# Kernel optimization log

Hardware: AMD Instinct MI355X
Metric: run time of the kernel (lower is better)

The kernel has to match this reference:

```python
import jax, jax.numpy as jnp
import numpy as np

N = 50000      # nodes
E = 800000     # edges (before self-loops)
F_IN = 64      # num_features
HID = 32       # hidden_channels
HEADS = 4
CLS = 3
NEG_SLOPE = 0.2  # PyG GATConv default


def setup_inputs() -> dict:
    key = jax.random.key(0)
    ks = jax.random.split(key, 12)
    s = 0.1
    return {
        "x": jax.random.normal(ks[0], (N, F_IN), jnp.float32),
        "W1": jax.random.normal(ks[1], (F_IN, HEADS * HID), jnp.float32) * s,
        "att_src1": jax.random.normal(ks[2], (HEADS, HID), jnp.float32) * s,
        "att_dst1": jax.random.normal(ks[3], (HEADS, HID), jnp.float32) * s,
        "b1": jnp.zeros((HEADS * HID,), jnp.float32),
        "W2": jax.random.normal(ks[4], (HEADS * HID, HID), jnp.float32) * s,
        "att_src2": jax.random.normal(ks[5], (1, HID), jnp.float32) * s,
        "att_dst2": jax.random.normal(ks[6], (1, HID), jnp.float32) * s,
        "b2": jnp.zeros((HID,), jnp.float32),
        "linW": jax.random.normal(ks[7], (HID, CLS), jnp.float32) * s,
        "linb": jnp.zeros((CLS,), jnp.float32),
        "edge_index": jax.random.randint(ks[8], (2, E), 0, N, dtype=jnp.int64),
    }


def _gat_conv(x, W, att_src, att_dst, bias, src, dst, heads):
    """PyG GATConv (eval mode, self-loops pre-added in src/dst)."""
    n = x.shape[0]
    h = (x @ W).reshape(n, heads, -1)                      # [N,H,C]
    a_src = jnp.sum(h * att_src, axis=-1)                  # [N,H]
    a_dst = jnp.sum(h * att_dst, axis=-1)                  # [N,H]
    e = jax.nn.leaky_relu(a_src[src] + a_dst[dst], NEG_SLOPE)  # [E,H]
    # segment softmax over destination node
    m = jax.ops.segment_max(e, dst, num_segments=n)
    p = jnp.exp(e - m[dst])
    denom = jax.ops.segment_sum(p, dst, num_segments=n)
    alpha = p / denom[dst]                                 # [E,H]
    msg = h[src] * alpha[:, :, None]                       # [E,H,C]
    out = jax.ops.segment_sum(msg, dst, num_segments=n)    # [N,H,C]
    return out.reshape(n, -1) + bias                       # concat heads


def reference(x, W1, att_src1, att_dst1, b1, W2, att_src2, att_dst2, b2, linW, linb, edge_index):
    n = x.shape[0]
    loop = jnp.arange(n, dtype=edge_index.dtype)
    src = jnp.concatenate([edge_index[0], loop])  # add self-loops (PyG default)
    dst = jnp.concatenate([edge_index[1], loop])
    h = _gat_conv(x, W1, att_src1, att_dst1, b1, src, dst, HEADS)
    h = jax.nn.elu(h)
    h = _gat_conv(h, W2, att_src2, att_dst2, b2, src, dst, 1)
    g = jnp.mean(h, axis=0, keepdims=True)        # batch is None path
    logits = g @ linW + linb                      # [1, CLS]
    return jax.nn.softmax(logits, axis=1)
```

## Files before the change

### kernel.cpp

```cpp
#include <hip/hip_runtime.h>
#include <hip/hip_fp16.h>
#include <math.h>

#define NEG_SLOPE 0.2f
#define CAP 64
#define SCB 2048

static __device__ __forceinline__ void atomAdd(float* a, float v) {
    unsafeAtomicAdd(a, v);
}

static __device__ __forceinline__ bool edges_are_i64(const int* __restrict__ ei) {
    return (ei[1] | ei[3] | ei[5] | ei[7]) == 0;
}
static __device__ __forceinline__ int ldsrc(const int* __restrict__ ei, int e, int E, bool i64) {
    return i64 ? ei[2 * e] : ei[e];
}
static __device__ __forceinline__ int lddst(const int* __restrict__ ei, int e, int E, bool i64) {
    return i64 ? ei[2 * (E + e)] : ei[E + e];
}

__global__ __launch_bounds__(256) void scatter_k(const int* __restrict__ ei,
                                                 int* __restrict__ deg,
                                                 int* __restrict__ col, int E, int N) {
    const int tid = threadIdx.x;
    const int grp = blockIdx.x & 3;
    const int bin = blockIdx.x >> 2;
    const int nb  = gridDim.x >> 2;
    const bool i64 = edges_are_i64(ei);
    const int ET = E + N;
    const int d0 = (int)((long long)grp * N / 4);
    const int d1 = (int)((long long)(grp + 1) * N / 4);
    for (int e = bin * 256 + tid; e < ET; e += nb * 256) {
        int s, d;
        if (e < E) { s = ldsrc(ei, e, E, i64); d = lddst(ei, e, E, i64); }
        else       { s = d = e - E; }
        if (d >= d0 && d < d1) {
            int pos = atomicAdd(&deg[d], 1);
            if (pos < CAP) col[d * CAP + pos] = s;
        }
    }
}

__global__ __launch_bounds__(256, 4) void gemm1_k(const float* __restrict__ x,
                                                  const float* __restrict__ W,
                                                  const float* __restrict__ aws,
                                                  const float* __restrict__ awd,
                                                  __half* __restrict__ h,
                                                  float* __restrict__ as_,
                                                  float* __restrict__ ad_, int N) {
    __shared__ float Ws[64 * 128];
    __shared__ float xs[32 * 64];
    const int tid = threadIdx.x;
    const int cg = tid & 31, rg = tid >> 5;
    const int r0 = blockIdx.x * 32;
#pragma unroll 1
    for (int i = tid; i < 8192; i += 256) Ws[i] = W[i];
    {
        const float* src = x + (size_t)r0 * 64;
        const int limit = (N - r0) * 64;
#pragma unroll 1
        for (int i = tid * 4; i < 2048; i += 1024) {
            float4 v = (i < limit) ? *(const float4*)(src + i) : make_float4(0, 0, 0, 0);
            *(float4*)(xs + i) = v;
        }
    }
    __syncthreads();

    float acc[4][4] = {};
#pragma unroll 2
    for (int k = 0; k < 64; k += 4) {
        float4 w0 = *(const float4*)(Ws + (k + 0) * 128 + cg * 4);
        float4 w1 = *(const float4*)(Ws + (k + 1) * 128 + cg * 4);
        float4 w2 = *(const float4*)(Ws + (k + 2) * 128 + cg * 4);
        float4 w3 = *(const float4*)(Ws + (k + 3) * 128 + cg * 4);
        float4 xv[4];
#pragma unroll
        for (int q = 0; q < 4; ++q) xv[q] = *(const float4*)(xs + (rg * 4 + q) * 64 + k);
#pragma unroll
        for (int q = 0; q < 4; ++q) {
            float4 xq = xv[q];
            acc[q][0] += xq.x * w0.x + xq.y * w1.x + xq.z * w2.x + xq.w * w3.x;
            acc[q][1] += xq.x * w0.y + xq.y * w1.y + xq.z * w2.y + xq.w * w3.y;
            acc[q][2] += xq.x * w0.z + xq.y * w1.z + xq.z * w2.z + xq.w * w3.z;
            acc[q][3] += xq.x * w0.w + xq.y * w1.w + xq.z * w2.w + xq.w * w3.w;
        }
    }

    const int jbase = cg * 4;
    const int head = cg >> 3;
    const float a0 = aws[jbase], a1 = aws[jbase + 1], a2 = aws[jbase + 2], a3 = aws[jbase + 3];
    const float d0 = awd[jbase], d1 = awd[jbase + 1], d2 = awd[jbase + 2], d3 = awd[jbase + 3];
    float ps[4], pd[4];
#pragma unroll
    for (int q = 0; q < 4; ++q) {
        ps[q] = acc[q][0] * a0 + acc[q][1] * a1 + acc[q][2] * a2 + acc[q][3] * a3;
        pd[q] = acc[q][0] * d0 + acc[q][1] * d1 + acc[q][2] * d2 + acc[q][3] * d3;
        int row = r0 + rg * 4 + q;
        if (row < N) {
            __half hv[4];
            hv[0] = __float2half(acc[q][0]); hv[1] = __float2half(acc[q][1]);
            hv[2] = __float2half(acc[q][2]); hv[3] = __float2half(acc[q][3]);
            *(uint2*)(h + (size_t)row * 128 + jbase) = *(uint2*)hv;
        }
    }
#pragma unroll
    for (int off = 4; off; off >>= 1) {
#pragma unroll
        for (int q = 0; q < 4; ++q) {
            ps[q] += __shfl_down(ps[q], off, 8);
            pd[q] += __shfl_down(pd[q], off, 8);
        }
    }
    if ((cg & 7) == 0) {
#pragma unroll
        for (int q = 0; q < 4; ++q) {
            int row = r0 + rg * 4 + q;
            if (row < N) { as_[row * 4 + head] = ps[q]; ad_[row * 4 + head] = pd[q]; }
        }
    }
}

__global__ __launch_bounds__(256, 4) void gemm2_k(const float* __restrict__ hact,
                                                  const float* __restrict__ W,
                                                  const float* __restrict__ aws,
                                                  const float* __restrict__ awd,
                                                  __half* __restrict__ h2,
                                                  float* __restrict__ as_,
                                                  float* __restrict__ ad_, int N) {
    __shared__ float Ws[128 * 32];
    __shared__ float xs[128 * 68];
    const int tid = threadIdx.x;
    const int cg = tid & 7, rg = tid >> 3;
    const int r0 = blockIdx.x * 128;
    for (int i = tid; i < 4096; i += 256) Ws[i] = W[i];

    float acc[4][4] = {};
#pragma unroll 1
    for (int p = 0; p < 2; ++p) {
        __syncthreads();
#pragma unroll 2
        for (int i = tid * 4; i < 8192; i += 1024) {
            int row = i >> 6, kk = i & 63;
            float4 v = (r0 + row < N)
                ? *(const float4*)(hact + (size_t)(r0 + row) * 128 + p * 64 + kk)
                : make_float4(0, 0, 0, 0);
            *(float4*)(xs + row * 68 + kk) = v;
        }
        __syncthreads();
#pragma unroll 2
        for (int k = 0; k < 64; k += 4) {
            float4 w0 = *(const float4*)(Ws + (p * 64 + k + 0) * 32 + cg * 4);
            float4 w1 = *(const float4*)(Ws + (p * 64 + k + 1) * 32 + cg * 4);
            float4 w2 = *(const float4*)(Ws + (p * 64 + k + 2) * 32 + cg * 4);
            float4 w3 = *(const float4*)(Ws + (p * 64 + k + 3) * 32 + cg * 4);
            float4 xv[4];
#pragma unroll
            for (int q = 0; q < 4; ++q) xv[q] = *(const float4*)(xs + (rg * 4 + q) * 68 + k);
#pragma unroll
            for (int q = 0; q < 4; ++q) {
                float4 xq = xv[q];
                acc[q][0] += xq.x * w0.x + xq.y * w1.x + xq.z * w2.x + xq.w * w3.x;
                acc[q][1] += xq.x * w0.y + xq.y * w1.y + xq.z * w2.y + xq.w * w3.y;
                acc[q][2] += xq.x * w0.z + xq.y * w1.z + xq.z * w2.z + xq.w * w3.z;
                acc[q][3] += xq.x * w0.w + xq.y * w1.w + xq.z * w2.w + xq.w * w3.w;
            }
        }
    }

    const int jbase = cg * 4;
    const float a0 = aws[jbase], a1 = aws[jbase + 1], a2 = aws[jbase + 2], a3 = aws[jbase + 3];
    const float d0 = awd[jbase], d1 = awd[jbase + 1], d2 = awd[jbase + 2], d3 = awd[jbase + 3];
    float ps[4], pd[4];
#pragma unroll
    for (int q = 0; q < 4; ++q) {
        ps[q] = acc[q][0] * a0 + acc[q][1] * a1 + acc[q][2] * a2 + acc[q][3] * a3;
        pd[q] = acc[q][0] * d0 + acc[q][1] * d1 + acc[q][2] * d2 + acc[q][3] * d3;
        int row = r0 + rg * 4 + q;
        if (row < N) {
            __half hv[4];
            hv[0] = __float2half(acc[q][0]); hv[1] = __float2half(acc[q][1]);
            hv[2] = __float2half(acc[q][2]); hv[3] = __float2half(acc[q][3]);
            *(uint2*)(h2 + (size_t)row * 32 + jbase) = *(uint2*)hv;
        }
    }
#pragma unroll
    for (int off = 4; off; off >>= 1) {
#pragma unroll
        for (int q = 0; q < 4; ++q) {
            ps[q] += __shfl_down(ps[q], off, 8);
            pd[q] += __shfl_down(pd[q], off, 8);
        }
    }
    if (cg == 0) {
#pragma unroll
        for (int q = 0; q < 4; ++q) {
            int row = r0 + rg * 4 + q;
            if (row < N) { as_[row] = ps[q]; ad_[row] = pd[q]; }
        }
    }
}

__global__ __launch_bounds__(256) void pull_agg1_k(const int* __restrict__ deg,
                                                   const int* __restrict__ col,
                                                   const float* __restrict__ asrc,
                                                   const float* __restrict__ adst,
                                                   const __half* __restrict__ h,
                                                   const float* __restrict__ b1,
                                                   float* __restrict__ hact, int N) {
    int wave = (blockIdx.x * 256 + threadIdx.x) >> 6;
    int lane = threadIdx.x & 63;
    if (wave >= N) return;
    const int d = wave;
    const int hd = lane >> 4;
    const int el = lane & 15;
    const float ad = adst[d * 4 + hd];
    const int* cl = col + d * CAP;
    int cnt = deg[d]; if (cnt > CAP) cnt = CAP;
    float acc0 = 0.0f, acc1 = 0.0f, den = 0.0f;

    for (int i = 0; i < cnt; i += 16) {
        const int r = cnt - i;
        int s = 0; float p = 0.0f;
        if (el < r) {
            s = cl[i + el];
            float v = asrc[s * 4 + hd] + ad;
            v = v > 0.0f ? v : NEG_SLOPE * v;
            p = __expf(v);
        }
        den += p;
        int su[16];
#pragma unroll
        for (int u = 0; u < 16; ++u) su[u] = __shfl(s, u, 16);
        __half2 g[16];
#pragma unroll
        for (int u = 0; u < 16; ++u) g[u] = *(const __half2*)(h + (size_t)su[u] * 128 + lane * 2);
        float pu[16];
#pragma unroll
        for (int u = 0; u < 16; ++u) pu[u] = __shfl(p, u, 16);
#pragma unroll
        for (int u = 0; u < 16; ++u) {
            float2 gf = __half22float2(g[u]);
            acc0 += pu[u] * gf.x; acc1 += pu[u] * gf.y;
        }
    }
    den += __shfl_xor(den, 1, 16);
    den += __shfl_xor(den, 2, 16);
    den += __shfl_xor(den, 4, 16);
    den += __shfl_xor(den, 8, 16);

    float inv = 1.0f / den;
    float o0 = acc0 * inv + b1[lane * 2];
    float o1 = acc1 * inv + b1[lane * 2 + 1];
    o0 = o0 > 0.0f ? o0 : expm1f(o0);
    o1 = o1 > 0.0f ? o1 : expm1f(o1);
    *(float2*)(hact + (size_t)d * 128 + lane * 2) = make_float2(o0, o1);
}

__global__ __launch_bounds__(256) void pull_agg2_k(const int* __restrict__ deg,
                                                   const int* __restrict__ col,
                                                   const float* __restrict__ asrc,
                                                   const float* __restrict__ adst,
                                                   const __half* __restrict__ h,
                                                   float* __restrict__ gsum, int N) {
    const int lane = threadIdx.x & 31;
    const int el = lane & 15;
    const int gloc = threadIdx.x >> 5;
    float csum = 0.0f;
    for (int d = blockIdx.x * 8 + gloc; d < N; d += gridDim.x * 8) {
        const float ad = adst[d];
        const int* cl = col + d * CAP;
        int cnt = deg[d]; if (cnt > CAP) cnt = CAP;
        float acc = 0.0f, den = 0.0f;
        for (int i = 0; i < cnt; i += 16) {
            const int r = cnt - i;
            int s = 0; float p = 0.0f;
            if (el < r) {
                s = cl[i + el];
                float v = asrc[s] + ad;
                v = v > 0.0f ? v : NEG_SLOPE * v;
                p = __expf(v);
            }
            den += p;
            int su[16];
#pragma unroll
            for (int u = 0; u < 16; ++u) su[u] = __shfl(s, u, 16);
            __half gg[16];
#pragma unroll
            for (int u = 0; u < 16; ++u) gg[u] = h[(size_t)su[u] * 32 + lane];
            float pu[16];
#pragma unroll
            for (int u = 0; u < 16; ++u) pu[u] = __shfl(p, u, 16);
#pragma unroll
            for (int u = 0; u < 16; ++u) acc += pu[u] * __half2float(gg[u]);
        }
        den += __shfl_xor(den, 1, 16);
        den += __shfl_xor(den, 2, 16);
        den += __shfl_xor(den, 4, 16);
        den += __shfl_xor(den, 8, 16);
        csum += acc / den;
    }
    __shared__ float lds[256];
    lds[threadIdx.x] = csum;
    __syncthreads();
    if (threadIdx.x < 32) {
        float s2 = 0.0f;
#pragma unroll
        for (int g = 0; g < 8; ++g) s2 += lds[g * 32 + threadIdx.x];
        atomAdd(&gsum[threadIdx.x], s2);
    }
}

__global__ void final_k(const float* __restrict__ gsum, const float* __restrict__ b2w,
                        const float* __restrict__ linW, const float* __restrict__ linb,
                        float* __restrict__ out, int N) {
    if (threadIdx.x != 0 || blockIdx.x != 0) return;
    float g[32];
#pragma unroll
    for (int c = 0; c < 32; ++c) g[c] = gsum[c] / (float)N + b2w[c];
    float lo[3];
#pragma unroll
    for (int j = 0; j < 3; ++j) {
        float acc = linb[j];
#pragma unroll
        for (int c = 0; c < 32; ++c) acc += g[c] * linW[c * 3 + j];
        lo[j] = acc;
    }
    float mx = fmaxf(lo[0], fmaxf(lo[1], lo[2]));
    float ex[3], se = 0.0f;
#pragma unroll
    for (int j = 0; j < 3; ++j) { ex[j] = __expf(lo[j] - mx); se += ex[j]; }
#pragma unroll
    for (int j = 0; j < 3; ++j) out[j] = ex[j] / se;
}

extern "C" void kernel_launch(void* const* d_in, const int* in_sizes, int n_in,
                              void* d_out, int out_size, void* d_ws, size_t ws_size,
                              hipStream_t stream) {
    const float* x    = (const float*)d_in[0];
    const float* W1   = (const float*)d_in[1];
    const float* as1w = (const float*)d_in[2];
    const float* ad1w = (const float*)d_in[3];
    const float* b1   = (const float*)d_in[4];
    const float* W2   = (const float*)d_in[5];
    const float* as2w = (const float*)d_in[6];
    const float* ad2w = (const float*)d_in[7];
    const float* b2w  = (const float*)d_in[8];
    const float* linW = (const float*)d_in[9];
    const float* linb = (const float*)d_in[10];
    const int*   ei   = (const int*)d_in[11];

    const int N = in_sizes[0] / 64;
    const int E = in_sizes[11] / 2;

    float* ws = (float*)d_ws;
    __half* h1h  = (__half*)ws;
    float*  hact = ws + (size_t)N * 64;
    float* asrc1 = hact + (size_t)N * 128;
    float* adst1 = asrc1 + (size_t)N * 4;
    float* asrc2 = adst1 + (size_t)N * 4;
    float* adst2 = asrc2 + (size_t)N;
    float* gsum  = adst2 + (size_t)N;
    __half* h2h  = (__half*)ws;
    int* deg     = (int*)(gsum + 32);
    int* col     = deg + N;

    auto cdiv = [](int a, int b) { return (a + b - 1) / b; };

    hipMemsetAsync(deg, 0, (size_t)N * sizeof(int), stream);
    hipMemsetAsync(gsum, 0, 32 * sizeof(float), stream);

    scatter_k<<<SCB, 256, 0, stream>>>(ei, deg, col, E, N);

    gemm1_k<<<cdiv(N, 32), 256, 0, stream>>>(x, W1, as1w, ad1w, h1h, asrc1, adst1, N);
    pull_agg1_k<<<cdiv(N, 4), 256, 0, stream>>>(deg, col, asrc1, adst1, h1h, b1, hact, N);

    gemm2_k<<<cdiv(N, 128), 256, 0, stream>>>(hact, W2, as2w, ad2w, h2h, asrc2, adst2, N);
    pull_agg2_k<<<2048, 256, 0, stream>>>(deg, col, asrc2, adst2, h2h, gsum, N);

    final_k<<<1, 64, 0, stream>>>(gsum, b2w, linW, linb, (float*)d_out, N);
}
```

Baseline: 241.8 us.

## Fuse layer-1 aggregation with layer-2 GEMM and attention projections

Merges the first-layer pull aggregation (with ELU) and the second-layer linear transform into one kernel. Each wave's aggregated 128-wide row is kept in shared memory and multiplied by a transposed W2 held in LDS, which removes the N×128 fp32 hact round-trip through global memory and one kernel launch. The two memsets are also merged into one contiguous memset. In exchange, every block of 8 nodes reloads and transposes all of W2 into LDS, and the 512-thread blocks with a larger LDS footprint may lower occupancy for the gather.

```diff
diff --git a/kernel.cpp b/kernel.cpp
--- a/kernel.cpp
+++ b/kernel.cpp
@@ -121,140 +121,117 @@
     }
 }
 
-__global__ __launch_bounds__(256, 4) void gemm2_k(const float* __restrict__ hact,
-                                                  const float* __restrict__ W,
-                                                  const float* __restrict__ aws,
-                                                  const float* __restrict__ awd,
-                                                  __half* __restrict__ h2,
-                                                  float* __restrict__ as_,
-                                                  float* __restrict__ ad_, int N) {
-    __shared__ float Ws[128 * 32];
-    __shared__ float xs[128 * 68];
+template <int NB>
+static __device__ __forceinline__ void p1_batch(int s, float p, const __half* __restrict__ h,
+                                                int lane, float& acc0, float& acc1) {
+    int su[NB];
+#pragma unroll
+    for (int u = 0; u < NB; ++u) su[u] = __shfl(s, u, 16);
+    __half2 g[NB];
+#pragma unroll
+    for (int u = 0; u < NB; ++u) g[u] = *(const __half2*)(h + (size_t)su[u] * 128 + lane * 2);
+    float pu[NB];
+#pragma unroll
+    for (int u = 0; u < NB; ++u) pu[u] = __shfl(p, u, 16);
+#pragma unroll
+    for (int u = 0; u < NB; ++u) {
+        float2 gf = __half22float2(g[u]);
+        acc0 += pu[u] * gf.x; acc1 += pu[u] * gf.y;
+    }
+}
+
+__global__ __launch_bounds__(512) void pg1_k(const int* __restrict__ deg,
+                                             const int* __restrict__ col,
+                                             const float* __restrict__ asrc,
+                                             const float* __restrict__ adst,
+                                             const __half* __restrict__ h,
+                                             const float* __restrict__ b1,
+                                             const float* __restrict__ W2,
+                                             const float* __restrict__ aws2,
+                                             const float* __restrict__ awd2,
+                                             __half* __restrict__ h2,
+                                             float* __restrict__ as2_,
+                                             float* __restrict__ ad2_, int N) {
+    __shared__ float W2t[32 * 132];
+    __shared__ float hrow[8][128];
     const int tid = threadIdx.x;
-    const int cg = tid & 7, rg = tid >> 3;
-    const int r0 = blockIdx.x * 128;
-    for (int i = tid; i < 4096; i += 256) Ws[i] = W[i];
-
-    float acc[4][4] = {};
-#pragma unroll 1
-    for (int p = 0; p < 2; ++p) {
-        __syncthreads();
-#pragma unroll 2
-        for (int i = tid * 4; i < 8192; i += 1024) {
-            int row = i >> 6, kk = i & 63;
-            float4 v = (r0 + row < N)
-                ? *(const float4*)(hact + (size_t)(r0 + row) * 128 + p * 64 + kk)
-                : make_float4(0, 0, 0, 0);
-            *(float4*)(xs + row * 68 + kk) = v;
-        }
-        __syncthreads();
-#pragma unroll 2
-        for (int k = 0; k < 64; k += 4) {
-            float4 w0 = *(const float4*)(Ws + (p * 64 + k + 0) * 32 + cg * 4);
-            float4 w1 = *(const float4*)(Ws + (p * 64 + k + 1) * 32 + cg * 4);
-            float4 w2 = *(const float4*)(Ws + (p * 64 + k + 2) * 32 + cg * 4);
-            float4 w3 = *(const float4*)(Ws + (p * 64 + k + 3) * 32 + cg * 4);
-            float4 xv[4];
-#pragma unroll
-            for (int q = 0; q < 4; ++q) xv[q] = *(const float4*)(xs + (rg * 4 + q) * 68 + k);
-#pragma unroll
-            for (int q = 0; q < 4; ++q) {
-                float4 xq = xv[q];
-                acc[q][0] += xq.x * w0.x + xq.y * w1.x + xq.z * w2.x + xq.w * w3.x;
-                acc[q][1] += xq.x * w0.y + xq.y * w1.y + xq.z * w2.y + xq.w * w3.y;
-                acc[q][2] += xq.x * w0.z + xq.y * w1.z + xq.z * w2.z + xq.w * w3.z;
-                acc[q][3] += xq.x * w0.w + xq.y * w1.w + xq.z * w2.w + xq.w * w3.w;
-            }
-        }
-    }
-
-    const int jbase = cg * 4;
-    const float a0 = aws[jbase], a1 = aws[jbase + 1], a2 = aws[jbase + 2], a3 = aws[jbase + 3];
-    const float d0 = awd[jbase], d1 = awd[jbase + 1], d2 = awd[jbase + 2], d3 = awd[jbase + 3];
-    float ps[4], pd[4];
-#pragma unroll
-    for (int q = 0; q < 4; ++q) {
-        ps[q] = acc[q][0] * a0 + acc[q][1] * a1 + acc[q][2] * a2 + acc[q][3] * a3;
-        pd[q] = acc[q][0] * d0 + acc[q][1] * d1 + acc[q][2] * d2 + acc[q][3] * d3;
-        int row = r0 + rg * 4 + q;
-        if (row < N) {
-            __half hv[4];
-            hv[0] = __float2half(acc[q][0]); hv[1] = __float2half(acc[q][1]);
-            hv[2] = __float2half(acc[q][2]); hv[3] = __float2half(acc[q][3]);
-            *(uint2*)(h2 + (size_t)row * 32 + jbase) = *(uint2*)hv;
-        }
-    }
-#pragma unroll
-    for (int off = 4; off; off >>= 1) {
-#pragma unroll
-        for (int q = 0; q < 4; ++q) {
-            ps[q] += __shfl_down(ps[q], off, 8);
-            pd[q] += __shfl_down(pd[q], off, 8);
-        }
-    }
-    if (cg == 0) {
-#pragma unroll
-        for (int q = 0; q < 4; ++q) {
-            int row = r0 + rg * 4 + q;
-            if (row < N) { as_[row] = ps[q]; ad_[row] = pd[q]; }
-        }
-    }
-}
-
-__global__ __launch_bounds__(256) void pull_agg1_k(const int* __restrict__ deg,
-                                                   const int* __restrict__ col,
-                                                   const float* __restrict__ asrc,
-                                                   const float* __restrict__ adst,
-                                                   const __half* __restrict__ h,
-                                                   const float* __restrict__ b1,
-                                                   float* __restrict__ hact, int N) {
-    int wave = (blockIdx.x * 256 + threadIdx.x) >> 6;
-    int lane = threadIdx.x & 63;
-    if (wave >= N) return;
-    const int d = wave;
+    for (int i = tid; i < 4096; i += 512) {
+        int k = i >> 5, j = i & 31;
+        W2t[j * 132 + k] = W2[i];
+    }
+    const int w = tid >> 6;
+    const int lane = tid & 63;
+    const int d = blockIdx.x * 8 + w;
     const int hd = lane >> 4;
     const int el = lane & 15;
-    const float ad = adst[d * 4 + hd];
-    const int* cl = col + d * CAP;
-    int cnt = deg[d]; if (cnt > CAP) cnt = CAP;
-    float acc0 = 0.0f, acc1 = 0.0f, den = 0.0f;
-
-    for (int i = 0; i < cnt; i += 16) {
-        const int r = cnt - i;
-        int s = 0; float p = 0.0f;
-        if (el < r) {
-            s = cl[i + el];
-            float v = asrc[s * 4 + hd] + ad;
-            v = v > 0.0f ? v : NEG_SLOPE * v;
-            p = __expf(v);
-        }
-        den += p;
-        int su[16];
-#pragma unroll
-        for (int u = 0; u < 16; ++u) su[u] = __shfl(s, u, 16);
-        __half2 g[16];
-#pragma unroll
-        for (int u = 0; u < 16; ++u) g[u] = *(const __half2*)(h + (size_t)su[u] * 128 + lane * 2);
-        float pu[16];
-#pragma unroll
-        for (int u = 0; u < 16; ++u) pu[u] = __shfl(p, u, 16);
-#pragma unroll
-        for (int u = 0; u < 16; ++u) {
-            float2 gf = __half22float2(g[u]);
-            acc0 += pu[u] * gf.x; acc1 += pu[u] * gf.y;
-        }
-    }
-    den += __shfl_xor(den, 1, 16);
-    den += __shfl_xor(den, 2, 16);
-    den += __shfl_xor(den, 4, 16);
-    den += __shfl_xor(den, 8, 16);
-
-    float inv = 1.0f / den;
-    float o0 = acc0 * inv + b1[lane * 2];
-    float o1 = acc1 * inv + b1[lane * 2 + 1];
-    o0 = o0 > 0.0f ? o0 : expm1f(o0);
-    o1 = o1 > 0.0f ? o1 : expm1f(o1);
-    *(float2*)(hact + (size_t)d * 128 + lane * 2) = make_float2(o0, o1);
+    if (d < N) {
+        const float ad = adst[d * 4 + hd];
+        const int* cl = col + d * CAP;
+        int cnt = deg[d]; if (cnt > CAP) cnt = CAP;
+        float acc0 = 0.0f, acc1 = 0.0f, den = 0.0f;
+        for (int i = 0; i < cnt; i += 16) {
+            const int r = cnt - i;
+            int s = 0; float p = 0.0f;
+            if (el < r) {
+                s = cl[i + el];
+                float v = asrc[s * 4 + hd] + ad;
+                v = v > 0.0f ? v : NEG_SLOPE * v;
+                p = __expf(v);
+            }
+            den += p;
+            p1_batch<16>(s, p, h, lane, acc0, acc1);
+        }
+        den += __shfl_xor(den, 1, 16);
+        den += __shfl_xor(den, 2, 16);
+        den += __shfl_xor(den, 4, 16);
+        den += __shfl_xor(den, 8, 16);
+        float inv = 1.0f / den;
+        float o0 = acc0 * inv + b1[lane * 2];
+        float o1 = acc1 * inv + b1[lane * 2 + 1];
+        o0 = o0 > 0.0f ? o0 : expm1f(o0);
+        o1 = o1 > 0.0f ? o1 : expm1f(o1);
+        hrow[w][lane * 2]     = o0;
+        hrow[w][lane * 2 + 1] = o1;
+    }
+    __syncthreads();
+    if (d < N) {
+        const int j = lane & 31, hf = lane >> 5;
+        const float4* hr4 = (const float4*)(hrow[w] + hf * 64);
+        const float*  wt  = W2t + j * 132 + hf * 64;
+        float sum = 0.0f;
+#pragma unroll
+        for (int k4 = 0; k4 < 16; ++k4) {
+            float4 hv = hr4[k4];
+            float4 wv = *(const float4*)(wt + k4 * 4);
+            sum += hv.x * wv.x + hv.y * wv.y + hv.z * wv.z + hv.w * wv.w;
+        }
+        sum += __shfl_xor(sum, 32, 64);
+        if (lane < 32) h2[(size_t)d * 32 + j] = __float2half(sum);
+        float t = sum * aws2[j];
+        float u = sum * awd2[j];
+#pragma unroll
+        for (int off = 16; off; off >>= 1) {
+            t += __shfl_xor(t, off, 32);
+            u += __shfl_xor(u, off, 32);
+        }
+        if (lane == 0) { as2_[d] = t; ad2_[d] = u; }
+    }
+}
+
+template <int NB>
+static __device__ __forceinline__ void p2_batch(int s, float p, const __half* __restrict__ h,
+                                                int lane, float& acc) {
+    int su[NB];
+#pragma unroll
+    for (int u = 0; u < NB; ++u) su[u] = __shfl(s, u, 16);
+    __half g[NB];
+#pragma unroll
+    for (int u = 0; u < NB; ++u) g[u] = h[(size_t)su[u] * 32 + lane];
+    float pu[NB];
+#pragma unroll
+    for (int u = 0; u < NB; ++u) pu[u] = __shfl(p, u, 16);
+#pragma unroll
+    for (int u = 0; u < NB; ++u) acc += pu[u] * __half2float(g[u]);
 }
 
 __global__ __launch_bounds__(256) void pull_agg2_k(const int* __restrict__ deg,
@@ -263,9 +240,10 @@
                                                    const float* __restrict__ adst,
                                                    const __half* __restrict__ h,
                                                    float* __restrict__ gsum, int N) {
-    const int lane = threadIdx.x & 31;
+    const int tid = threadIdx.x;
+    const int lane = tid & 31;
     const int el = lane & 15;
-    const int gloc = threadIdx.x >> 5;
+    const int gloc = tid >> 5;
     float csum = 0.0f;
     for (int d = blockIdx.x * 8 + gloc; d < N; d += gridDim.x * 8) {
         const float ad = adst[d];
@@ -282,17 +260,7 @@
                 p = __expf(v);
             }
             den += p;
-            int su[16];
-#pragma unroll
-            for (int u = 0; u < 16; ++u) su[u] = __shfl(s, u, 16);
-            __half gg[16];
-#pragma unroll
-            for (int u = 0; u < 16; ++u) gg[u] = h[(size_t)su[u] * 32 + lane];
-            float pu[16];
-#pragma unroll
-            for (int u = 0; u < 16; ++u) pu[u] = __shfl(p, u, 16);
-#pragma unroll
-            for (int u = 0; u < 16; ++u) acc += pu[u] * __half2float(gg[u]);
+            p2_batch<16>(s, p, h, lane, acc);
         }
         den += __shfl_xor(den, 1, 16);
         den += __shfl_xor(den, 2, 16);
@@ -301,13 +269,13 @@
         csum += acc / den;
     }
     __shared__ float lds[256];
-    lds[threadIdx.x] = csum;
+    lds[tid] = csum;
     __syncthreads();
-    if (threadIdx.x < 32) {
+    if (tid < 32) {
         float s2 = 0.0f;
 #pragma unroll
-        for (int g = 0; g < 8; ++g) s2 += lds[g * 32 + threadIdx.x];
-        atomAdd(&gsum[threadIdx.x], s2);
+        for (int g = 0; g < 8; ++g) s2 += lds[g * 32 + tid];
+        atomAdd(&gsum[tid], s2);
     }
 }
 
@@ -355,27 +323,26 @@
 
     float* ws = (float*)d_ws;
     __half* h1h  = (__half*)ws;
-    float*  hact = ws + (size_t)N * 64;
-    float* asrc1 = hact + (size_t)N * 128;
+    float* asrc1 = ws + (size_t)N * 64;
     float* adst1 = asrc1 + (size_t)N * 4;
-    float* asrc2 = adst1 + (size_t)N * 4;
+    __half* h2h  = (__half*)(adst1 + (size_t)N * 4);
+    float* asrc2 = adst1 + (size_t)N * 4 + (size_t)N * 16;
     float* adst2 = asrc2 + (size_t)N;
     float* gsum  = adst2 + (size_t)N;
-    __half* h2h  = (__half*)ws;
     int* deg     = (int*)(gsum + 32);
     int* col     = deg + N;
 
     auto cdiv = [](int a, int b) { return (a + b - 1) / b; };
 
-    hipMemsetAsync(deg, 0, (size_t)N * sizeof(int), stream);
-    hipMemsetAsync(gsum, 0, 32 * sizeof(float), stream);
+    hipMemsetAsync(gsum, 0, (size_t)(32 + N) * sizeof(int), stream);
 
     scatter_k<<<SCB, 256, 0, stream>>>(ei, deg, col, E, N);
 
     gemm1_k<<<cdiv(N, 32), 256, 0, stream>>>(x, W1, as1w, ad1w, h1h, asrc1, adst1, N);
-    pull_agg1_k<<<cdiv(N, 4), 256, 0, stream>>>(deg, col, asrc1, adst1, h1h, b1, hact, N);
-
-    gemm2_k<<<cdiv(N, 128), 256, 0, stream>>>(hact, W2, as2w, ad2w, h2h, asrc2, adst2, N);
+
+    pg1_k<<<cdiv(N, 8), 512, 0, stream>>>(deg, col, asrc1, adst1, h1h, b1,
+                                          W2, as2w, ad2w, h2h, asrc2, adst2, N);
+
     pull_agg2_k<<<2048, 256, 0, stream>>>(deg, col, asrc2, adst2, h2h, gsum, N);
 
     final_k<<<1, 64, 0, stream>>>(gsum, b2w, linW, linb, (float*)d_out, N);
```

Result: slower. 252.5 us (+4.4%).
